# Optimization experiments

Hardware: AMD Instinct MI355X
Metric: run time of the kernel (lower is better)

The kernel has to match this reference:

```python
import jax, jax.numpy as jnp
import numpy as np

B, T, H, V = 4, 1024, 1024, 32000
IGNORE_INDEX = -100
BETA = 0.1


def setup_inputs() -> dict:
    key = jax.random.key(0)
    k1, k2, k3, k4, k5, k6 = jax.random.split(key, 6)
    x = jax.random.normal(k1, (B, T, H), dtype=jnp.float32)
    ref_x = jax.random.normal(k2, (B, T, H), dtype=jnp.float32)
    y = jax.random.randint(k3, (B, T), 0, V, dtype=jnp.int64)
    preference_labels = jax.random.randint(k4, (B,), 0, 2) > 0
    scale = 1.0 / np.sqrt(H)
    W = jax.random.normal(k5, (V, H), dtype=jnp.float32) * scale
    ref_W = jax.random.normal(k6, (V, H), dtype=jnp.float32) * scale
    return {"x": x, "ref_x": ref_x, "y": y, "preference_labels": preference_labels, "W": W, "ref_W": ref_W}


def _avg_logps(h, W, y):
    # h: [B,T,H], W: [V,H], y: [B,T] -> per-example mean target log-prob [B]
    logits = jnp.einsum("bth,vh->btv", h, W)
    logp = jax.nn.log_softmax(logits.astype(jnp.float32), axis=-1)
    mask = y != IGNORE_INDEX
    labels = jnp.where(mask, y, 0)
    per_tok = jnp.take_along_axis(logp, labels[..., None], axis=-1)[..., 0]  # [B,T]
    return (per_tok * mask).sum(-1) / mask.sum(-1)


def reference(x, ref_x, y, preference_labels, W, ref_W):
    policy_logps = _avg_logps(x, W, y)                                   # [B]
    ref_logps = jax.lax.stop_gradient(_avg_logps(ref_x, ref_W, y))       # reference model: no grad
    logratios = policy_logps - ref_logps
    kl = jnp.zeros((), dtype=jnp.float32)  # kl=None path in Liger KTO
    chosen = 1.0 - jax.nn.sigmoid(BETA * (logratios - kl))
    rejected = 1.0 - jax.nn.sigmoid(BETA * (kl - logratios))
    losses = jnp.where(preference_labels, chosen, rejected)
    return losses.sum() / y.shape[0]
```

## Files before the change

### kernel.cpp

```cpp
#include <hip/hip_runtime.h>
#include <hip/hip_bf16.h>

#define MROWS 4096
#define KDIM 1024
#define NVOCAB 32000
#define MTILES (MROWS / 128)
#define NTILES (NVOCAB / 128)
#define NCH 250
#define KT 16
#define BETA 0.1f
#define WSCALE 32.0f
#define INVWSCALE 0.03125f
#define M0 8.0f

typedef __attribute__((ext_vector_type(4))) int i4v;
typedef __attribute__((ext_vector_type(8))) int i8v;
typedef __attribute__((ext_vector_type(16))) float f16v;

__device__ inline unsigned q4(float f) {
  float af = fabsf(f);
  unsigned idx = (af >= 0.25f) + (af >= 0.75f) + (af >= 1.25f) + (af >= 1.75f)
               + (af >= 2.5f) + (af >= 3.5f) + (af >= 5.0f);
  return idx | (f < 0.f ? 8u : 0u);
}

__global__ void cvt_all(const float4* __restrict__ x, const float4* __restrict__ rx,
                        const float4* __restrict__ W, const float4* __restrict__ rW,
                        unsigned* __restrict__ xq, unsigned* __restrict__ rxq,
                        unsigned* __restrict__ Wq, unsigned* __restrict__ rWq) {
  const int NA = MTILES * KT * 1024;
  const int NW = NTILES * KT * 1024;
  const int total = 2 * NA + 2 * NW;
  for (int g = blockIdx.x * 256 + threadIdx.x; g < total; g += gridDim.x * 256) {
    const float4* s; unsigned* d; int j; float sc;
    if (g < NA)               { s = x;  d = xq;  j = g;               sc = 1.f; }
    else if (g < 2 * NA)      { s = rx; d = rxq; j = g - NA;          sc = 1.f; }
    else if (g < 2 * NA + NW) { s = W;  d = Wq;  j = g - 2 * NA;      sc = WSCALE; }
    else                      { s = rW; d = rWq; j = g - 2 * NA - NW; sc = WSCALE; }
    const int tile = j >> 14;
    const int rem  = j & 16383;
    const int step = rem >> 10;
    const int c    = rem & 1023;
    const int blk = c >> 8, r = c & 255;
    const int l = r >> 2, u = r & 3;
    const int row = tile * 128 + blk * 32 + (l & 31);
    const int kbase = step * 64 + (l >> 5) * 32 + u * 8;
    const float4* p = s + ((size_t)row * KDIM + kbase) / 4;
    float4 a = p[0], b = p[1];
    unsigned o = q4(a.x * sc)        | (q4(a.y * sc) << 4)
               | (q4(a.z * sc) << 8) | (q4(a.w * sc) << 12)
               | (q4(b.x * sc) << 16)| (q4(b.y * sc) << 20)
               | (q4(b.z * sc) << 24)| (q4(b.w * sc) << 28);
    d[j] = o;
  }
}

__device__ inline i8v ldfrag(const unsigned char* p) {
  i4v lo = *(const i4v*)p;
  return __builtin_shufflevector(lo, lo, 0, 1, 2, 3, -1, -1, -1, -1);
}

__global__ __launch_bounds__(64, 2) void gemm_lse(
    const unsigned char* __restrict__ xq, const unsigned char* __restrict__ rxq,
    const unsigned char* __restrict__ Wq, const unsigned char* __restrict__ rWq,
    const int* __restrict__ y,
    float* __restrict__ partials,
    float* __restrict__ tgt)
{
  const int bid = blockIdx.x;
  const int bz  = blockIdx.y;
  const int xcd = bid & 7;
  const int idx = bid >> 3;
  const int n128 = idx >> 3;
  const int m64  = xcd * 8 + (idx & 7);
  const int m0 = m64 * 64, n0 = n128 * 128;

  const unsigned char* Ap = (bz ? rxq : xq) + (size_t)(m64 >> 1) * (KT * 4096)
                            + (m64 & 1) * 2048;
  const unsigned char* Bp = (bz ? rWq : Wq) + (size_t)n128 * (KT * 4096);

  const int lane = threadIdx.x;
  const int l31 = lane & 31, hi5 = lane >> 5;

  const unsigned char* pa = Ap + lane * 16;
  const unsigned char* pb = Bp + lane * 16;

  f16v acc[2][4];
#pragma unroll
  for (int i = 0; i < 2; ++i)
#pragma unroll
    for (int j = 0; j < 4; ++j) acc[i][j] = (f16v)(0.f);

#pragma unroll 2
  for (int s = 0; s < KT; ++s) {
    i8v a0 = ldfrag(pa);
    i8v a1 = ldfrag(pa + 1024);
    i8v b0 = ldfrag(pb);
    i8v b1 = ldfrag(pb + 1024);
    i8v b2 = ldfrag(pb + 2048);
    i8v b3 = ldfrag(pb + 3072);
    acc[0][0] = __builtin_amdgcn_mfma_scale_f32_32x32x64_f8f6f4(a0, b0, acc[0][0], 4, 4, 0, 127, 0, 127);
    acc[0][1] = __builtin_amdgcn_mfma_scale_f32_32x32x64_f8f6f4(a0, b1, acc[0][1], 4, 4, 0, 127, 0, 127);
    acc[0][2] = __builtin_amdgcn_mfma_scale_f32_32x32x64_f8f6f4(a0, b2, acc[0][2], 4, 4, 0, 127, 0, 127);
    acc[0][3] = __builtin_amdgcn_mfma_scale_f32_32x32x64_f8f6f4(a0, b3, acc[0][3], 4, 4, 0, 127, 0, 127);
    acc[1][0] = __builtin_amdgcn_mfma_scale_f32_32x32x64_f8f6f4(a1, b0, acc[1][0], 4, 4, 0, 127, 0, 127);
    acc[1][1] = __builtin_amdgcn_mfma_scale_f32_32x32x64_f8f6f4(a1, b1, acc[1][1], 4, 4, 0, 127, 0, 127);
    acc[1][2] = __builtin_amdgcn_mfma_scale_f32_32x32x64_f8f6f4(a1, b2, acc[1][2], 4, 4, 0, 127, 0, 127);
    acc[1][3] = __builtin_amdgcn_mfma_scale_f32_32x32x64_f8f6f4(a1, b3, acc[1][3], 4, 4, 0, 127, 0, 127);
    pa += 4096;
    pb += 4096;
  }

  int yreg = y[m0 + lane];
#pragma unroll
  for (int mi = 0; mi < 2; ++mi) {
#pragma unroll
    for (int r = 0; r < 16; ++r) {
      float v0 = acc[mi][0][r] * INVWSCALE, v1 = acc[mi][1][r] * INVWSCALE;
      float v2 = acc[mi][2][r] * INVWSCALE, v3 = acc[mi][3][r] * INVWSCALE;
      float ex = __expf(v0 - M0) + __expf(v1 - M0) + __expf(v2 - M0) + __expf(v3 - M0);
#pragma unroll
      for (int d = 1; d < 32; d <<= 1) ex += __shfl_xor(ex, d);
      int rowInBlock = mi * 32 + (r & 3) + 8 * (r >> 2) + 4 * hi5;
      int grow = m0 + rowInBlock;
      if (l31 == 0)
        partials[((size_t)bz * NCH + n128) * MROWS + grow] = ex;
      int yv = __shfl(yreg, rowInBlock);
      int cl = yv - n0;
      if (cl >= 0 && cl < 128 && (cl & 31) == l31) {
        int ni = cl >> 5;
        float tv = ni == 0 ? v0 : ni == 1 ? v1 : ni == 2 ? v2 : v3;
        tgt[(size_t)bz * MROWS + grow] = tv;
      }
    }
  }
}

__global__ void rowred(const float* __restrict__ partials, const float* __restrict__ tgt,
                       const int* __restrict__ y, float* __restrict__ sums) {
  const int model = blockIdx.x >> 4;
  const int rb = blockIdx.x & 15;
  const int row = rb * 256 + threadIdx.x;
  const int b = row >> 10;
  const float* p = partials + (size_t)model * NCH * MROWS + row;
  float s0 = 0.f, s1 = 0.f, s2 = 0.f, s3 = 0.f;
#pragma unroll 4
  for (int j = 0; j < NCH; j += 4) {
    s0 += p[(size_t)j * MROWS];
    s1 += p[(size_t)(j + 1) * MROWS];
    s2 += p[(size_t)(j + 2) * MROWS];
    s3 += p[(size_t)(j + 3) * MROWS];
  }
  float S = (s0 + s1) + (s2 + s3);
  int yv = y[row];
  float val = 0.f, c = 0.f;
  if (yv != -100) {
    val = tgt[(size_t)model * MROWS + row] - (M0 + __logf(S));
    c = 1.f;
  }
#pragma unroll
  for (int d = 1; d < 64; d <<= 1) { val += __shfl_xor(val, d); c += __shfl_xor(c, d); }
  __shared__ float sv[4], sc[4];
  const int w = threadIdx.x >> 6;
  if ((threadIdx.x & 63) == 0) { sv[w] = val; sc[w] = c; }
  __syncthreads();
  if (threadIdx.x == 0) {
    float s = sv[0] + sv[1] + sv[2] + sv[3];
    float cc = sc[0] + sc[1] + sc[2] + sc[3];
    atomicAdd(&sums[model * 4 + b], s);
    atomicAdd(&sums[8 + model * 4 + b], cc);
  }
}

__global__ void finalk(const float* __restrict__ sums, const int* __restrict__ pref,
                       float* __restrict__ out) {
  if (threadIdx.x == 0 && blockIdx.x == 0) {
    float acc = 0.f;
    for (int b = 0; b < 4; ++b) {
      float lp = sums[b] / sums[8 + b];
      float lr = sums[4 + b] / sums[12 + b];
      float z = BETA * (lp - lr);
      float sig = 1.f / (1.f + __expf(-z));
      acc += (pref[b] != 0) ? (1.f - sig) : sig;
    }
    out[0] = acc * 0.25f;
  }
}

extern "C" void kernel_launch(void* const* d_in, const int* in_sizes, int n_in,
                              void* d_out, int out_size, void* d_ws, size_t ws_size,
                              hipStream_t stream) {
  const float* x    = (const float*)d_in[0];
  const float* rx   = (const float*)d_in[1];
  const int*   y    = (const int*)d_in[2];
  const int*   pref = (const int*)d_in[3];
  const float* W    = (const float*)d_in[4];
  const float* rW   = (const float*)d_in[5];
  float* out = (float*)d_out;

  char* ws = (char*)d_ws;
  const size_t SZ_X = (size_t)MROWS * KDIM / 2;
  const size_t SZ_W = (size_t)NVOCAB * KDIM / 2;
  unsigned char* xq  = (unsigned char*)(ws);
  unsigned char* rxq = (unsigned char*)(ws + SZ_X);
  unsigned char* Wq  = (unsigned char*)(ws + 2 * SZ_X);
  unsigned char* rWq = (unsigned char*)(ws + 2 * SZ_X + SZ_W);
  float* partials = (float*)(ws + 2 * SZ_X + 2 * SZ_W);
  float* tgt      = (float*)(ws + 2 * SZ_X + 2 * SZ_W + (size_t)2 * NCH * MROWS * 4);
  float* sums     = (float*)(ws + 2 * SZ_X + 2 * SZ_W + (size_t)2 * NCH * MROWS * 4 + 2 * MROWS * 4);

  cvt_all<<<dim3(2048), 256, 0, stream>>>((const float4*)x, (const float4*)rx,
                                          (const float4*)W, (const float4*)rW,
                                          (unsigned*)xq, (unsigned*)rxq,
                                          (unsigned*)Wq, (unsigned*)rWq);

  hipMemsetAsync(sums, 0, 16 * sizeof(float), stream);

  gemm_lse<<<dim3(16000, 2), 64, 0, stream>>>(xq, rxq, Wq, rWq, y, partials, tgt);
  rowred<<<dim3(32), 256, 0, stream>>>(partials, tgt, y, sums);
  finalk<<<dim3(1), 64, 0, stream>>>(sums, pref, out);
}
```

Measured before the change: 296.1 us.

## Accumulate row exp-sums with atomics and raise MFMA wave priority

The GEMM epilogue now adds each row's partial exp-sum straight into a per-row accumulator with atomicAdd, replacing the per-vocab-chunk partials buffer. The row reduction kernel then reads a single value per row instead of 250, which removes roughly 8 MB of partial writes and reads. s_setprio is also raised around the MFMA block so waves that are issuing matrix work get scheduling priority. The cost is heavy atomic contention, since each row receives 250 atomic adds. The sums buffer is now written directly, so its memset is dropped and rowsum is memset instead.

```diff
diff --git a/kernel.cpp b/kernel.cpp
--- a/kernel.cpp
+++ b/kernel.cpp
@@ -6,7 +6,6 @@
 #define NVOCAB 32000
 #define MTILES (MROWS / 128)
 #define NTILES (NVOCAB / 128)
-#define NCH 250
 #define KT 16
 #define BETA 0.1f
 #define WSCALE 32.0f
@@ -64,7 +63,7 @@
     const unsigned char* __restrict__ xq, const unsigned char* __restrict__ rxq,
     const unsigned char* __restrict__ Wq, const unsigned char* __restrict__ rWq,
     const int* __restrict__ y,
-    float* __restrict__ partials,
+    float* __restrict__ rowsum,
     float* __restrict__ tgt)
 {
   const int bid = blockIdx.x;
@@ -99,6 +98,7 @@
     i8v b1 = ldfrag(pb + 1024);
     i8v b2 = ldfrag(pb + 2048);
     i8v b3 = ldfrag(pb + 3072);
+    __builtin_amdgcn_s_setprio(1);
     acc[0][0] = __builtin_amdgcn_mfma_scale_f32_32x32x64_f8f6f4(a0, b0, acc[0][0], 4, 4, 0, 127, 0, 127);
     acc[0][1] = __builtin_amdgcn_mfma_scale_f32_32x32x64_f8f6f4(a0, b1, acc[0][1], 4, 4, 0, 127, 0, 127);
     acc[0][2] = __builtin_amdgcn_mfma_scale_f32_32x32x64_f8f6f4(a0, b2, acc[0][2], 4, 4, 0, 127, 0, 127);
@@ -107,6 +107,7 @@
     acc[1][1] = __builtin_amdgcn_mfma_scale_f32_32x32x64_f8f6f4(a1, b1, acc[1][1], 4, 4, 0, 127, 0, 127);
     acc[1][2] = __builtin_amdgcn_mfma_scale_f32_32x32x64_f8f6f4(a1, b2, acc[1][2], 4, 4, 0, 127, 0, 127);
     acc[1][3] = __builtin_amdgcn_mfma_scale_f32_32x32x64_f8f6f4(a1, b3, acc[1][3], 4, 4, 0, 127, 0, 127);
+    __builtin_amdgcn_s_setprio(0);
     pa += 4096;
     pb += 4096;
   }
@@ -124,7 +125,7 @@
       int rowInBlock = mi * 32 + (r & 3) + 8 * (r >> 2) + 4 * hi5;
       int grow = m0 + rowInBlock;
       if (l31 == 0)
-        partials[((size_t)bz * NCH + n128) * MROWS + grow] = ex;
+        atomicAdd(&rowsum[(size_t)bz * MROWS + grow], ex);
       int yv = __shfl(yreg, rowInBlock);
       int cl = yv - n0;
       if (cl >= 0 && cl < 128 && (cl & 31) == l31) {
@@ -136,22 +137,12 @@
   }
 }
 
-__global__ void rowred(const float* __restrict__ partials, const float* __restrict__ tgt,
+__global__ void rowred(const float* __restrict__ rowsum, const float* __restrict__ tgt,
                        const int* __restrict__ y, float* __restrict__ sums) {
-  const int model = blockIdx.x >> 4;
-  const int rb = blockIdx.x & 15;
-  const int row = rb * 256 + threadIdx.x;
-  const int b = row >> 10;
-  const float* p = partials + (size_t)model * NCH * MROWS + row;
-  float s0 = 0.f, s1 = 0.f, s2 = 0.f, s3 = 0.f;
-#pragma unroll 4
-  for (int j = 0; j < NCH; j += 4) {
-    s0 += p[(size_t)j * MROWS];
-    s1 += p[(size_t)(j + 1) * MROWS];
-    s2 += p[(size_t)(j + 2) * MROWS];
-    s3 += p[(size_t)(j + 3) * MROWS];
-  }
-  float S = (s0 + s1) + (s2 + s3);
+  const int model = blockIdx.x >> 2;
+  const int b = blockIdx.x & 3;
+  const int row = b * 1024 + threadIdx.x;
+  float S = rowsum[(size_t)model * MROWS + row];
   int yv = y[row];
   float val = 0.f, c = 0.f;
   if (yv != -100) {
@@ -160,15 +151,16 @@
   }
 #pragma unroll
   for (int d = 1; d < 64; d <<= 1) { val += __shfl_xor(val, d); c += __shfl_xor(c, d); }
-  __shared__ float sv[4], sc[4];
+  __shared__ float sv[16], sc[16];
   const int w = threadIdx.x >> 6;
   if ((threadIdx.x & 63) == 0) { sv[w] = val; sc[w] = c; }
   __syncthreads();
   if (threadIdx.x == 0) {
-    float s = sv[0] + sv[1] + sv[2] + sv[3];
-    float cc = sc[0] + sc[1] + sc[2] + sc[3];
-    atomicAdd(&sums[model * 4 + b], s);
-    atomicAdd(&sums[8 + model * 4 + b], cc);
+    float s = 0.f, cc = 0.f;
+#pragma unroll
+    for (int i = 0; i < 16; ++i) { s += sv[i]; cc += sc[i]; }
+    sums[model * 4 + b] = s;
+    sums[8 + model * 4 + b] = cc;
   }
 }
 
@@ -205,18 +197,18 @@
   unsigned char* rxq = (unsigned char*)(ws + SZ_X);
   unsigned char* Wq  = (unsigned char*)(ws + 2 * SZ_X);
   unsigned char* rWq = (unsigned char*)(ws + 2 * SZ_X + SZ_W);
-  float* partials = (float*)(ws + 2 * SZ_X + 2 * SZ_W);
-  float* tgt      = (float*)(ws + 2 * SZ_X + 2 * SZ_W + (size_t)2 * NCH * MROWS * 4);
-  float* sums     = (float*)(ws + 2 * SZ_X + 2 * SZ_W + (size_t)2 * NCH * MROWS * 4 + 2 * MROWS * 4);
+  float* rowsum = (float*)(ws + 2 * SZ_X + 2 * SZ_W);
+  float* tgt    = (float*)(ws + 2 * SZ_X + 2 * SZ_W + 2 * MROWS * 4);
+  float* sums   = (float*)(ws + 2 * SZ_X + 2 * SZ_W + 4 * MROWS * 4);
 
   cvt_all<<<dim3(2048), 256, 0, stream>>>((const float4*)x, (const float4*)rx,
                                           (const float4*)W, (const float4*)rW,
                                           (unsigned*)xq, (unsigned*)rxq,
                                           (unsigned*)Wq, (unsigned*)rWq);
 
-  hipMemsetAsync(sums, 0, 16 * sizeof(float), stream);
-
-  gemm_lse<<<dim3(16000, 2), 64, 0, stream>>>(xq, rxq, Wq, rWq, y, partials, tgt);
-  rowred<<<dim3(32), 256, 0, stream>>>(partials, tgt, y, sums);
+  hipMemsetAsync(rowsum, 0, 2 * MROWS * sizeof(float), stream);
+
+  gemm_lse<<<dim3(16000, 2), 64, 0, stream>>>(xq, rxq, Wq, rWq, y, rowsum, tgt);
+  rowred<<<dim3(8), 1024, 0, stream>>>(rowsum, tgt, y, sums);
   finalk<<<dim3(1), 64, 0, stream>>>(sums, pref, out);
 }
```

After: 296.5 us. No clear change (+0.1%).
